# Performance work log

Hardware: AMD Instinct MI355X
Metric: run time of the kernel (lower is better)

Reference implementation:

```python
import jax, jax.numpy as jnp
import numpy as np
import math

S, B, D = 1024, 8, 512
H = 8
HD = D // H
DFF = 2048
NUM_BUCKETS = 32
MAX_DISTANCE = 128
LN_EPS = 1e-5


def setup_inputs() -> dict:
    key = jax.random.key(0)
    ks = jax.random.split(key, 12)
    s = 0.02
    return {
        "x": jax.random.normal(ks[0], (S, B, D), jnp.float32),
        "attn_mask": jnp.zeros((S, S), jnp.float32),
        "in_proj_w": jax.random.normal(ks[1], (3 * D, D), jnp.float32) * s,
        "in_proj_b": jnp.zeros((3 * D,), jnp.float32),
        "out_proj_w": jax.random.normal(ks[2], (D, D), jnp.float32) * s,
        "out_proj_b": jnp.zeros((D,), jnp.float32),
        "lin1_w": jax.random.normal(ks[3], (DFF, D), jnp.float32) * s,
        "lin1_b": jnp.zeros((DFF,), jnp.float32),
        "lin2_w": jax.random.normal(ks[4], (D, DFF), jnp.float32) * s,
        "lin2_b": jnp.zeros((D,), jnp.float32),
        "ln1_w": jnp.ones((D,), jnp.float32),
        "ln1_b": jnp.zeros((D,), jnp.float32),
        "ln2_w": jnp.ones((D,), jnp.float32),
        "ln2_b": jnp.zeros((D,), jnp.float32),
        "rel_emb": jax.random.normal(ks[5], (NUM_BUCKETS, H), jnp.float32) * s,
    }


def _relative_position_bucket(relative_position, num_buckets=NUM_BUCKETS, max_distance=MAX_DISTANCE):
    # bidirectional=True path (encoder)
    nb = num_buckets // 2
    rel_buckets = (relative_position > 0).astype(jnp.int32) * nb
    rp = jnp.abs(relative_position)
    max_exact = nb // 2
    is_small = rp < max_exact
    rp_safe = jnp.maximum(rp, 1)  # avoid log(0); masked by is_small below
    rp_large = max_exact + (
        jnp.log(rp_safe.astype(jnp.float32) / max_exact)
        / math.log(max_distance / max_exact)
        * (nb - max_exact)
    ).astype(jnp.int32)
    rp_large = jnp.minimum(rp_large, nb - 1)
    return rel_buckets + jnp.where(is_small, rp, rp_large)


def _compute_bias(rel_emb, q_len, k_len):
    ctx = jnp.arange(q_len, dtype=jnp.int32)[:, None]
    mem = jnp.arange(k_len, dtype=jnp.int32)[None, :]
    buckets = _relative_position_bucket(mem - ctx)          # [S, S]
    values = rel_emb[buckets]                                # [S, S, H]
    return jnp.transpose(values, (2, 0, 1))                  # [H, S, S]


def _layer_norm(x, w, b):
    mu = jnp.mean(x, axis=-1, keepdims=True)
    var = jnp.mean(jnp.square(x - mu), axis=-1, keepdims=True)
    return (x - mu) * jax.lax.rsqrt(var + LN_EPS) * w + b


def reference(x, attn_mask, in_proj_w, in_proj_b, out_proj_w, out_proj_b,
              lin1_w, lin1_b, lin2_w, lin2_b, ln1_w, ln1_b, ln2_w, ln2_b, rel_emb):
    s, b, d = x.shape
    # qkv projection (torch Linear: y = x W^T + b)
    qkv = x @ in_proj_w.T + in_proj_b                         # [S, B, 3D]
    q, k, v = jnp.split(qkv, 3, axis=-1)

    def to_bhsd(t):
        return jnp.transpose(t.reshape(s, b, H, HD), (1, 2, 0, 3))  # [B, H, S, HD]

    q, k, v = to_bhsd(q), to_bhsd(k), to_bhsd(v)
    scores = jnp.einsum("bhqd,bhkd->bhqk", q, k) / math.sqrt(HD)

    bias = _compute_bias(rel_emb, s, s)                       # [H, S, S]
    mask_bias = attn_mask[None, :, :] + bias                  # [H, S, S]
    attn = jax.nn.softmax(scores + mask_bias[None], axis=-1)  # [B, H, S, S]

    o = jnp.einsum("bhqk,bhkd->bhqd", attn, v)                # [B, H, S, HD]
    o = jnp.transpose(o, (2, 0, 1, 3)).reshape(s, b, d)       # [S, B, D]
    o = o @ out_proj_w.T + out_proj_b

    # post-norm (norm_first=False)
    y = _layer_norm(x + o, ln1_w, ln1_b)
    ff = jax.nn.relu(y @ lin1_w.T + lin1_b) @ lin2_w.T + lin2_b
    return _layer_norm(y + ff, ln2_w, ln2_b)
```

## Files before the change

### kernel.cpp

```cpp
#include <hip/hip_runtime.h>
#include <hip/hip_bf16.h>


#define S_LEN 1024
#define BATCH 8
#define DMODEL 512
#define NHEAD 8
#define HDIM 64
#define DFF 2048
#define NROWS (S_LEN * BATCH)

typedef __bf16 bf16x8 __attribute__((ext_vector_type(8)));
typedef float f32x4 __attribute__((ext_vector_type(4)));

__device__ __forceinline__ void gload16(const void* g, void* l) {
    __builtin_amdgcn_global_load_lds(
        (const __attribute__((address_space(1))) void*)g,
        (__attribute__((address_space(3))) void*)l, 16, 0, 0);
}

__global__ __launch_bounds__(256)
void cast_kernel(const float* __restrict__ in, __hip_bfloat16* __restrict__ out, int n) {
    int i = (blockIdx.x * blockDim.x + threadIdx.x) * 4;
    if (i + 3 < n) {
        float4 v = *(const float4*)(in + i);
        out[i + 0] = __float2bfloat16(v.x);
        out[i + 1] = __float2bfloat16(v.y);
        out[i + 2] = __float2bfloat16(v.z);
        out[i + 3] = __float2bfloat16(v.w);
    }
}

__global__ void bias_table_kernel(const float* __restrict__ rel_emb,
                                  float* __restrict__ bias_tab) {
    int idx = blockIdx.x * blockDim.x + threadIdx.x;
    if (idx >= 2 * S_LEN - 1) return;
    int rel = idx - (S_LEN - 1);
    int bucket = (rel > 0) ? 16 : 0;
    int rp = rel < 0 ? -rel : rel;
    int v;
    if (rp < 8)          v = rp;
    else if (rp < 12)    v = 8;
    else if (rp < 16)    v = 9;
    else if (rp < 23)    v = 10;
    else if (rp < 32)    v = 11;
    else if (rp < 46)    v = 12;
    else if (rp < 64)    v = 13;
    else if (rp < 91)    v = 14;
    else                 v = 15;
    bucket += v;
    for (int h = 0; h < NHEAD; ++h)
        bias_tab[idx * NHEAD + h] = rel_emb[bucket * NHEAD + h];
}

__global__ __launch_bounds__(256)
void embc_kernel(const float* __restrict__ mask,
                 const float* __restrict__ bias_tab,
                 __hip_bfloat16* __restrict__ embC) {
    int tid = blockIdx.x * 256 + threadIdx.x;
    int h  = tid >> 16;
    int r1 = tid & 65535;
    int qt = r1 >> 12;
    int w  = (r1 >> 10) & 3;
    int kb = (r1 >> 6) & 15;
    int lane = r1 & 63;
    int qbase = qt * 64 + w * 16 + (lane >> 4) * 4;
    int kbase = kb * 64 + (lane & 15);
    __hip_bfloat16 ov[16];
#pragma unroll
    for (int j = 0; j < 16; ++j) {
        int c = j >> 2, e = j & 3;
        int q = qbase + e, k = kbase + c * 16;
        float m = mask[(size_t)q * S_LEN + k];
        float bt = bias_tab[(k - q + S_LEN - 1) * NHEAD + h];
        ov[j] = __float2bfloat16(__expf(m + bt));
    }
    *(uint4*)(embC + (size_t)tid * 16) = *(uint4*)&ov[0];
    *(uint4*)(embC + (size_t)tid * 16 + 8) = *(uint4*)&ov[8];
}

template <int MODE, bool RELU, int NTILE>
__global__ __launch_bounds__(256)
void gemm_tile(const __hip_bfloat16* __restrict__ Ab,
               const __hip_bfloat16* __restrict__ Wb,
               const float* __restrict__ bias,
               void* __restrict__ outv,
               int N, int M, int K) {
    constexpr int RT = (NTILE == 128) ? 4 : 2;
    constexpr int NB = NTILE / 32;
    const int w = threadIdx.x >> 6;
    const int lane = threadIdx.x & 63;
    const int m16 = lane & 15;
    const int quad = lane >> 4;
    const int row0 = blockIdx.y * 128;
    const int col0 = blockIdx.x * NTILE;
    const int rowbase = (NTILE == 128) ? (w >> 1) * 64 : w * 32;
    const int colbase = (NTILE == 128) ? (w & 1) * 64 : 0;

    __shared__ __align__(16) __bf16 As[128 * 64];
    __shared__ __align__(16) __bf16 Bs[NTILE * 64];

    const __bf16* Ap = (const __bf16*)Ab;
    const __bf16* Wp = (const __bf16*)Wb;

    const int a_row_in_grp = lane >> 3;
    const int kb_sw = (lane & 7) ^ (lane >> 3);

    f32x4 acc[4][RT];
#pragma unroll
    for (int c = 0; c < 4; ++c)
#pragma unroll
        for (int r = 0; r < RT; ++r) acc[c][r] = f32x4{0, 0, 0, 0};

    for (int k0 = 0; k0 < K; k0 += 64) {
#pragma unroll
        for (int i = 0; i < 4; ++i) {
            int grp = w * 4 + i;
            int row = grp * 8 + a_row_in_grp;
            gload16(Ap + (size_t)(row0 + row) * K + k0 + kb_sw * 8,
                    (void*)(As + grp * 512));
        }
#pragma unroll
        for (int i = 0; i < NB; ++i) {
            int grp = w * NB + i;
            int row = grp * 8 + a_row_in_grp;
            gload16(Wp + (size_t)(col0 + row) * K + k0 + kb_sw * 8,
                    (void*)(Bs + grp * 512));
        }
        __syncthreads();

#pragma unroll
        for (int kk = 0; kk < 2; ++kk) {
            bf16x8 af[RT], bfr[4];
#pragma unroll
            for (int r = 0; r < RT; ++r) {
                int rr = rowbase + r * 16 + m16;
                int slot = (kk * 4 + quad) ^ (m16 & 7);
                af[r] = *(const bf16x8*)(As + rr * 64 + slot * 8);
            }
#pragma unroll
            for (int c = 0; c < 4; ++c) {
                int rr = colbase + c * 16 + m16;
                int slot = (kk * 4 + quad) ^ (m16 & 7);
                bfr[c] = *(const bf16x8*)(Bs + rr * 64 + slot * 8);
            }
#pragma unroll
            for (int c = 0; c < 4; ++c)
#pragma unroll
                for (int r = 0; r < RT; ++r)
                    acc[c][r] = __builtin_amdgcn_mfma_f32_16x16x32_bf16(
                        af[r], bfr[c], acc[c][r], 0, 0, 0);
        }
        __syncthreads();
    }

#pragma unroll
    for (int c = 0; c < 4; ++c) {
        int col = col0 + colbase + c * 16 + m16;
        float bv = bias[col];
#pragma unroll
        for (int r = 0; r < RT; ++r) {
#pragma unroll
            for (int e = 0; e < 4; ++e) {
                int row = row0 + rowbase + r * 16 + quad * 4 + e;
                float v = acc[c][r][e] + bv;
                if (RELU) v = fmaxf(v, 0.f);
                if (MODE == 0) {
                    ((float*)outv)[(size_t)row * M + col] = v;
                } else if (MODE == 1) {
                    ((__hip_bfloat16*)outv)[(size_t)row * M + col] = __float2bfloat16(v);
                } else {
                    int sect = col >> 9, h = (col >> 6) & 7, d = col & 63;
                    int s = row >> 3, bb = row & 7;
                    size_t idx;
                    if (sect == 2)
                        idx = (size_t)(128 + bb * 8 + h) * (S_LEN * HDIM)
                            + (size_t)d * S_LEN + s;
                    else
                        idx = ((size_t)(sect * 64 + bb * 8 + h) * S_LEN + s) * HDIM + d;
                    ((__hip_bfloat16*)outv)[idx] = __float2bfloat16(v);
                }
            }
        }
    }
}

__device__ __forceinline__ int p_addr(int r, int k) {
    return r * 64 + ((((k >> 3) ^ (r & 7))) << 3) + (k & 7);
}

__global__ __launch_bounds__(256, 4)
void attn_mfma(const __hip_bfloat16* __restrict__ qkv_bhsd,
               const __hip_bfloat16* __restrict__ embC,
               __hip_bfloat16* __restrict__ o) {
    const int bh = blockIdx.y;
    const int b = bh >> 3, h = bh & 7;
    const int qt = blockIdx.x;
    const int q0 = qt * 64;
    const int t = threadIdx.x;
    const int w = t >> 6, lane = t & 63, m16 = lane & 15, quad = lane >> 4;

    const __bf16* Qb  = (const __bf16*)qkv_bhsd + (size_t)bh * (S_LEN * HDIM);
    const __bf16* Kb  = (const __bf16*)qkv_bhsd + (size_t)(64 + bh) * (S_LEN * HDIM);
    const __bf16* VTg = (const __bf16*)qkv_bhsd + (size_t)(128 + bh) * (S_LEN * HDIM);
    const __hip_bfloat16* ec =
        embC + ((((size_t)h * 16 + qt) * 4 + w) * 16) * 1024 + (size_t)lane * 16;

    __shared__ __align__(16) __bf16 Ks[2][64 * 64];
    __shared__ __align__(16) __bf16 Vs[2][64 * 64];
    __shared__ __align__(16) __bf16 P[4][16 * 64];

    const int r_in = lane >> 3;
    const int kb_sw = (lane & 7) ^ r_in;

    auto stage = [&](int kc, int p) {
#pragma unroll
        for (int i = 0; i < 2; ++i) {
            int grp = w * 2 + i;
            gload16(Kb + (size_t)(kc + grp * 8 + r_in) * HDIM + kb_sw * 8,
                    (void*)(&Ks[p][grp * 512]));
            gload16(VTg + (size_t)(grp * 8 + r_in) * S_LEN + kc + kb_sw * 8,
                    (void*)(&Vs[p][grp * 512]));
        }
    };

    bf16x8 aQ0, aQ1;
    {
        const __bf16* qp = Qb + (size_t)(q0 + w * 16 + m16) * HDIM + quad * 8;
        bf16x8 t0 = *(const bf16x8*)qp;
        bf16x8 t1 = *(const bf16x8*)(qp + 32);
#pragma unroll
        for (int j = 0; j < 8; ++j) {
            t0[j] = (__bf16)((float)t0[j] * 0.125f);
            t1[j] = (__bf16)((float)t1[j] * 0.125f);
        }
        aQ0 = t0; aQ1 = t1;
    }

    f32x4 accO[4] = {f32x4{0,0,0,0}, f32x4{0,0,0,0}, f32x4{0,0,0,0}, f32x4{0,0,0,0}};
    float lpart[4] = {0.f, 0.f, 0.f, 0.f};

    stage(0, 0);
    __syncthreads();

    int p = 0;
    for (int kc = 0; kc < S_LEN; kc += 64, p ^= 1) {
        if (kc + 64 < S_LEN) stage(kc + 64, p ^ 1);

        union { uint4 u[2]; __hip_bfloat16 e[16]; } ev;
        ev.u[0] = *(const uint4*)(ec + (size_t)(kc >> 6) * 1024);
        ev.u[1] = *(const uint4*)(ec + (size_t)(kc >> 6) * 1024 + 8);

        f32x4 accS[4] = {f32x4{0,0,0,0}, f32x4{0,0,0,0}, f32x4{0,0,0,0}, f32x4{0,0,0,0}};
        const int sub = (m16 >> 3) * 512 + (m16 & 7) * 64;
        const int s0 = (quad ^ (m16 & 7)) * 8;
        const int s1 = ((4 + quad) ^ (m16 & 7)) * 8;
#pragma unroll
        for (int c = 0; c < 4; ++c) {
            const __bf16* kr = &Ks[p][c * 1024 + sub];
            bf16x8 b0 = *(const bf16x8*)(kr + s0);
            bf16x8 b1 = *(const bf16x8*)(kr + s1);
            accS[c] = __builtin_amdgcn_mfma_f32_16x16x32_bf16(aQ0, b0, accS[c], 0, 0, 0);
            accS[c] = __builtin_amdgcn_mfma_f32_16x16x32_bf16(aQ1, b1, accS[c], 0, 0, 0);
        }

#pragma unroll
        for (int c = 0; c < 4; ++c)
#pragma unroll
            for (int e = 0; e < 4; ++e) {
                float pv = __expf(accS[c][e]) * __bfloat162float(ev.e[c * 4 + e]);
                lpart[e] += pv;
                P[w][p_addr(quad * 4 + e, c * 16 + m16)] = (__bf16)pv;
            }

        bf16x8 aP0 = *(const bf16x8*)&P[w][p_addr(m16, quad * 8)];
        bf16x8 aP1 = *(const bf16x8*)&P[w][p_addr(m16, 32 + quad * 8)];
#pragma unroll
        for (int c = 0; c < 4; ++c) {
            const __bf16* vr = &Vs[p][c * 1024 + sub];
            bf16x8 v0 = *(const bf16x8*)(vr + s0);
            bf16x8 v1 = *(const bf16x8*)(vr + s1);
            accO[c] = __builtin_amdgcn_mfma_f32_16x16x32_bf16(aP0, v0, accO[c], 0, 0, 0);
            accO[c] = __builtin_amdgcn_mfma_f32_16x16x32_bf16(aP1, v1, accO[c], 0, 0, 0);
        }

        __syncthreads();
    }

    float lrow[4];
#pragma unroll
    for (int e = 0; e < 4; ++e) {
        float l = lpart[e];
#pragma unroll
        for (int off = 1; off < 16; off <<= 1) l += __shfl_xor(l, off);
        lrow[e] = 1.f / l;
    }

#pragma unroll
    for (int c = 0; c < 4; ++c)
#pragma unroll
        for (int e = 0; e < 4; ++e) {
            int row = q0 + w * 16 + quad * 4 + e;
            int d = c * 16 + m16;
            float v = accO[c][e] * lrow[e];
            o[((size_t)row * BATCH + b) * DMODEL + h * HDIM + d] = __float2bfloat16(v);
        }
}

__global__ __launch_bounds__(64)
void ln_kernel(const float* __restrict__ resid,
               const float* __restrict__ gin,
               const float* __restrict__ w,
               const float* __restrict__ b,
               float* __restrict__ outf,
               __hip_bfloat16* __restrict__ outb) {
    const int row = blockIdx.x;
    const int lane = threadIdx.x;
    const float* rp = resid + (size_t)row * DMODEL;
    const float* gp = gin + (size_t)row * DMODEL;

    float v[8];
    float s = 0.f, s2 = 0.f;
#pragma unroll
    for (int i = 0; i < 8; ++i) {
        int d = i * 64 + lane;
        float x = rp[d] + gp[d];
        v[i] = x;
        s += x;
        s2 += x * x;
    }
#pragma unroll
    for (int off = 32; off; off >>= 1) {
        s  += __shfl_xor(s, off);
        s2 += __shfl_xor(s2, off);
    }
    float mu = s * (1.f / DMODEL);
    float var = s2 * (1.f / DMODEL) - mu * mu;
    float rs = rsqrtf(var + 1e-5f);
#pragma unroll
    for (int i = 0; i < 8; ++i) {
        int d = i * 64 + lane;
        float y = (v[i] - mu) * rs * w[d] + b[d];
        outf[(size_t)row * DMODEL + d] = y;
        if (outb) outb[(size_t)row * DMODEL + d] = __float2bfloat16(y);
    }
}

extern "C" void kernel_launch(void* const* d_in, const int* in_sizes, int n_in,
                              void* d_out, int out_size, void* d_ws, size_t ws_size,
                              hipStream_t stream) {
    const float* x          = (const float*)d_in[0];
    const float* attn_mask  = (const float*)d_in[1];
    const float* in_proj_w  = (const float*)d_in[2];
    const float* in_proj_b  = (const float*)d_in[3];
    const float* out_proj_w = (const float*)d_in[4];
    const float* out_proj_b = (const float*)d_in[5];
    const float* lin1_w     = (const float*)d_in[6];
    const float* lin1_b     = (const float*)d_in[7];
    const float* lin2_w     = (const float*)d_in[8];
    const float* lin2_b     = (const float*)d_in[9];
    const float* ln1_w      = (const float*)d_in[10];
    const float* ln1_b      = (const float*)d_in[11];
    const float* ln2_w      = (const float*)d_in[12];
    const float* ln2_b      = (const float*)d_in[13];
    const float* rel_emb    = (const float*)d_in[14];

    char* ws = (char*)d_ws;
    size_t off = 0;
    auto alloc = [&](size_t bytes) {
        char* p = ws + off;
        off += (bytes + 255) / 256 * 256;
        return (void*)p;
    };
    float* bias_tab       = (float*)alloc((2 * S_LEN - 1) * NHEAD * 4);
    __hip_bfloat16* embt  = (__hip_bfloat16*)alloc((size_t)NHEAD * S_LEN * S_LEN * 2);
    __hip_bfloat16* wqkvb = (__hip_bfloat16*)alloc((size_t)3 * DMODEL * DMODEL * 2);
    __hip_bfloat16* wob   = (__hip_bfloat16*)alloc((size_t)DMODEL * DMODEL * 2);
    __hip_bfloat16* w1b   = (__hip_bfloat16*)alloc((size_t)DFF * DMODEL * 2);
    __hip_bfloat16* w2b   = (__hip_bfloat16*)alloc((size_t)DMODEL * DFF * 2);
    __hip_bfloat16* xb    = (__hip_bfloat16*)alloc((size_t)NROWS * DMODEL * 2);
    __hip_bfloat16* qkvb  = (__hip_bfloat16*)alloc((size_t)3 * 64 * S_LEN * HDIM * 2);
    __hip_bfloat16* o     = (__hip_bfloat16*)alloc((size_t)NROWS * DMODEL * 2);
    float* tmp            = (float*)alloc((size_t)NROWS * DMODEL * 4);
    float* yf             = (float*)alloc((size_t)NROWS * DMODEL * 4);
    __hip_bfloat16* yb    = (__hip_bfloat16*)alloc((size_t)NROWS * DMODEL * 2);
    __hip_bfloat16* ffb   = (__hip_bfloat16*)alloc((size_t)NROWS * DFF * 2);

    float* out = (float*)d_out;

    cast_kernel<<<dim3(3 * DMODEL * DMODEL / 1024), 256, 0, stream>>>(in_proj_w, wqkvb, 3 * DMODEL * DMODEL);
    cast_kernel<<<dim3(DMODEL * DMODEL / 1024), 256, 0, stream>>>(out_proj_w, wob, DMODEL * DMODEL);
    cast_kernel<<<dim3(DFF * DMODEL / 1024), 256, 0, stream>>>(lin1_w, w1b, DFF * DMODEL);
    cast_kernel<<<dim3(DMODEL * DFF / 1024), 256, 0, stream>>>(lin2_w, w2b, DMODEL * DFF);
    cast_kernel<<<dim3(NROWS * DMODEL / 1024), 256, 0, stream>>>(x, xb, NROWS * DMODEL);
    bias_table_kernel<<<dim3(8), 256, 0, stream>>>(rel_emb, bias_tab);
    embc_kernel<<<dim3(2048), 256, 0, stream>>>(attn_mask, bias_tab, embt);

    gemm_tile<2, false, 128><<<dim3(12, 64), 256, 0, stream>>>(
        xb, wqkvb, in_proj_b, qkvb, NROWS, 3 * DMODEL, DMODEL);

    attn_mfma<<<dim3(S_LEN / 64, BATCH * NHEAD), 256, 0, stream>>>(
        qkvb, embt, o);

    gemm_tile<0, false, 64><<<dim3(8, 64), 256, 0, stream>>>(
        o, wob, out_proj_b, tmp, NROWS, DMODEL, DMODEL);

    ln_kernel<<<dim3(NROWS), 64, 0, stream>>>(x, tmp, ln1_w, ln1_b, yf, yb);

    gemm_tile<1, true, 128><<<dim3(16, 64), 256, 0, stream>>>(
        yb, w1b, lin1_b, ffb, NROWS, DFF, DMODEL);

    gemm_tile<0, false, 64><<<dim3(8, 64), 256, 0, stream>>>(
        ffb, w2b, lin2_b, tmp, NROWS, DMODEL, DFF);

    ln_kernel<<<dim3(NROWS), 64, 0, stream>>>(yf, tmp, ln2_w, ln2_b, out, nullptr);
}
```

Measured before the change: 299.4 us.

## Fuse cast kernels, inline bias buckets, double-buffer narrow GEMMs, transpose attention MFMAs

Merges the five weight/input cast launches into one vectorized prep kernel and computes relative-position buckets directly inside the embC kernel, removing the bias table kernel. Adds a double-buffered 64-column GEMM for the out-projection and FFN2 so global-to-LDS loads overlap MFMA work. The attention kernel now computes transposed score and output tiles, so each lane owns one query row: the row-sum becomes a two-step shuffle, P writes are packed 4-wide, and output stores are vectorized. The double buffer doubles LDS use in the narrow GEMM, and the changed embC index mapping must still match the layout the attention kernel reads.

```diff
diff --git a/kernel.cpp b/kernel.cpp
--- a/kernel.cpp
+++ b/kernel.cpp
@@ -11,7 +11,8 @@
 #define NROWS (S_LEN * BATCH)
 
 typedef __bf16 bf16x8 __attribute__((ext_vector_type(8)));
-typedef float f32x4 __attribute__((ext_vector_type(4)));
+typedef short  s16x4  __attribute__((ext_vector_type(4)));
+typedef float  f32x4  __attribute__((ext_vector_type(4)));
 
 __device__ __forceinline__ void gload16(const void* g, void* l) {
     __builtin_amdgcn_global_load_lds(
@@ -20,42 +21,34 @@
 }
 
 __global__ __launch_bounds__(256)
-void cast_kernel(const float* __restrict__ in, __hip_bfloat16* __restrict__ out, int n) {
-    int i = (blockIdx.x * blockDim.x + threadIdx.x) * 4;
-    if (i + 3 < n) {
-        float4 v = *(const float4*)(in + i);
-        out[i + 0] = __float2bfloat16(v.x);
-        out[i + 1] = __float2bfloat16(v.y);
-        out[i + 2] = __float2bfloat16(v.z);
-        out[i + 3] = __float2bfloat16(v.w);
-    }
-}
-
-__global__ void bias_table_kernel(const float* __restrict__ rel_emb,
-                                  float* __restrict__ bias_tab) {
-    int idx = blockIdx.x * blockDim.x + threadIdx.x;
-    if (idx >= 2 * S_LEN - 1) return;
-    int rel = idx - (S_LEN - 1);
-    int bucket = (rel > 0) ? 16 : 0;
-    int rp = rel < 0 ? -rel : rel;
-    int v;
-    if (rp < 8)          v = rp;
-    else if (rp < 12)    v = 8;
-    else if (rp < 16)    v = 9;
-    else if (rp < 23)    v = 10;
-    else if (rp < 32)    v = 11;
-    else if (rp < 46)    v = 12;
-    else if (rp < 64)    v = 13;
-    else if (rp < 91)    v = 14;
-    else                 v = 15;
-    bucket += v;
-    for (int h = 0; h < NHEAD; ++h)
-        bias_tab[idx * NHEAD + h] = rel_emb[bucket * NHEAD + h];
+void prep_kernel(const float* __restrict__ x,
+                 const float* __restrict__ wq, const float* __restrict__ wo,
+                 const float* __restrict__ w1, const float* __restrict__ w2,
+                 __hip_bfloat16* __restrict__ xb, __hip_bfloat16* __restrict__ wqb,
+                 __hip_bfloat16* __restrict__ wob, __hip_bfloat16* __restrict__ w1b,
+                 __hip_bfloat16* __restrict__ w2b) {
+    const int NX = NROWS * DMODEL / 4;
+    const int NQ = 3 * DMODEL * DMODEL / 4;
+    const int NO = DMODEL * DMODEL / 4;
+    const int N1 = DFF * DMODEL / 4;
+    int i = blockIdx.x * 256 + threadIdx.x;
+    const float* src; __hip_bfloat16* dst; int off;
+    if (i < NX)                         { src = x;  dst = xb;  off = i; }
+    else if ((i -= NX) < NQ)            { src = wq; dst = wqb; off = i; }
+    else if ((i -= NQ) < NO)            { src = wo; dst = wob; off = i; }
+    else if ((i -= NO) < N1)            { src = w1; dst = w1b; off = i; }
+    else if ((i -= N1) < N1)            { src = w2; dst = w2b; off = i; }
+    else return;
+    float4 v = *(const float4*)(src + (size_t)off * 4);
+    union { s16x4 s; __hip_bfloat16 b[4]; } u;
+    u.b[0] = __float2bfloat16(v.x); u.b[1] = __float2bfloat16(v.y);
+    u.b[2] = __float2bfloat16(v.z); u.b[3] = __float2bfloat16(v.w);
+    *(s16x4*)(dst + (size_t)off * 4) = u.s;
 }
 
 __global__ __launch_bounds__(256)
 void embc_kernel(const float* __restrict__ mask,
-                 const float* __restrict__ bias_tab,
+                 const float* __restrict__ rel_emb,
                  __hip_bfloat16* __restrict__ embC) {
     int tid = blockIdx.x * 256 + threadIdx.x;
     int h  = tid >> 16;
@@ -64,41 +57,50 @@
     int w  = (r1 >> 10) & 3;
     int kb = (r1 >> 6) & 15;
     int lane = r1 & 63;
-    int qbase = qt * 64 + w * 16 + (lane >> 4) * 4;
-    int kbase = kb * 64 + (lane & 15);
+    int q = qt * 64 + w * 16 + (lane & 15);
     __hip_bfloat16 ov[16];
 #pragma unroll
     for (int j = 0; j < 16; ++j) {
         int c = j >> 2, e = j & 3;
-        int q = qbase + e, k = kbase + c * 16;
-        float m = mask[(size_t)q * S_LEN + k];
-        float bt = bias_tab[(k - q + S_LEN - 1) * NHEAD + h];
-        ov[j] = __float2bfloat16(__expf(m + bt));
+        int k = kb * 64 + c * 16 + (lane >> 4) * 4 + e;
+        int rel = k - q;
+        int bucket = (rel > 0) ? 16 : 0;
+        int rp = rel < 0 ? -rel : rel;
+        int v;
+        if (rp < 8)          v = rp;
+        else if (rp < 12)    v = 8;
+        else if (rp < 16)    v = 9;
+        else if (rp < 23)    v = 10;
+        else if (rp < 32)    v = 11;
+        else if (rp < 46)    v = 12;
+        else if (rp < 64)    v = 13;
+        else if (rp < 91)    v = 14;
+        else                 v = 15;
+        float bt = rel_emb[(bucket + v) * NHEAD + h];
+        ov[j] = __float2bfloat16(__expf(mask[(size_t)q * S_LEN + k] + bt));
     }
     *(uint4*)(embC + (size_t)tid * 16) = *(uint4*)&ov[0];
     *(uint4*)(embC + (size_t)tid * 16 + 8) = *(uint4*)&ov[8];
 }
 
-template <int MODE, bool RELU, int NTILE>
+template <int MODE, bool RELU>
 __global__ __launch_bounds__(256)
 void gemm_tile(const __hip_bfloat16* __restrict__ Ab,
                const __hip_bfloat16* __restrict__ Wb,
                const float* __restrict__ bias,
                void* __restrict__ outv,
                int N, int M, int K) {
-    constexpr int RT = (NTILE == 128) ? 4 : 2;
-    constexpr int NB = NTILE / 32;
     const int w = threadIdx.x >> 6;
     const int lane = threadIdx.x & 63;
     const int m16 = lane & 15;
     const int quad = lane >> 4;
     const int row0 = blockIdx.y * 128;
-    const int col0 = blockIdx.x * NTILE;
-    const int rowbase = (NTILE == 128) ? (w >> 1) * 64 : w * 32;
-    const int colbase = (NTILE == 128) ? (w & 1) * 64 : 0;
+    const int col0 = blockIdx.x * 128;
+    const int rowbase = (w >> 1) * 64;
+    const int colbase = (w & 1) * 64;
 
     __shared__ __align__(16) __bf16 As[128 * 64];
-    __shared__ __align__(16) __bf16 Bs[NTILE * 64];
+    __shared__ __align__(16) __bf16 Bs[128 * 64];
 
     const __bf16* Ap = (const __bf16*)Ab;
     const __bf16* Wp = (const __bf16*)Wb;
@@ -106,11 +108,11 @@
     const int a_row_in_grp = lane >> 3;
     const int kb_sw = (lane & 7) ^ (lane >> 3);
 
-    f32x4 acc[4][RT];
+    f32x4 acc[4][4];
 #pragma unroll
     for (int c = 0; c < 4; ++c)
 #pragma unroll
-        for (int r = 0; r < RT; ++r) acc[c][r] = f32x4{0, 0, 0, 0};
+        for (int r = 0; r < 4; ++r) acc[c][r] = f32x4{0, 0, 0, 0};
 
     for (int k0 = 0; k0 < K; k0 += 64) {
 #pragma unroll
@@ -119,11 +121,6 @@
             int row = grp * 8 + a_row_in_grp;
             gload16(Ap + (size_t)(row0 + row) * K + k0 + kb_sw * 8,
                     (void*)(As + grp * 512));
-        }
-#pragma unroll
-        for (int i = 0; i < NB; ++i) {
-            int grp = w * NB + i;
-            int row = grp * 8 + a_row_in_grp;
             gload16(Wp + (size_t)(col0 + row) * K + k0 + kb_sw * 8,
                     (void*)(Bs + grp * 512));
         }
@@ -131,23 +128,18 @@
 
 #pragma unroll
         for (int kk = 0; kk < 2; ++kk) {
-            bf16x8 af[RT], bfr[4];
-#pragma unroll
-            for (int r = 0; r < RT; ++r) {
-                int rr = rowbase + r * 16 + m16;
-                int slot = (kk * 4 + quad) ^ (m16 & 7);
-                af[r] = *(const bf16x8*)(As + rr * 64 + slot * 8);
-            }
-#pragma unroll
-            for (int c = 0; c < 4; ++c) {
-                int rr = colbase + c * 16 + m16;
-                int slot = (kk * 4 + quad) ^ (m16 & 7);
-                bfr[c] = *(const bf16x8*)(Bs + rr * 64 + slot * 8);
-            }
+            bf16x8 af[4], bfr[4];
+            int slot = (kk * 4 + quad) ^ (m16 & 7);
+#pragma unroll
+            for (int r = 0; r < 4; ++r)
+                af[r] = *(const bf16x8*)(As + (rowbase + r * 16 + m16) * 64 + slot * 8);
 #pragma unroll
             for (int c = 0; c < 4; ++c)
-#pragma unroll
-                for (int r = 0; r < RT; ++r)
+                bfr[c] = *(const bf16x8*)(Bs + (colbase + c * 16 + m16) * 64 + slot * 8);
+#pragma unroll
+            for (int c = 0; c < 4; ++c)
+#pragma unroll
+                for (int r = 0; r < 4; ++r)
                     acc[c][r] = __builtin_amdgcn_mfma_f32_16x16x32_bf16(
                         af[r], bfr[c], acc[c][r], 0, 0, 0);
         }
@@ -159,15 +151,13 @@
         int col = col0 + colbase + c * 16 + m16;
         float bv = bias[col];
 #pragma unroll
-        for (int r = 0; r < RT; ++r) {
+        for (int r = 0; r < 4; ++r) {
 #pragma unroll
             for (int e = 0; e < 4; ++e) {
                 int row = row0 + rowbase + r * 16 + quad * 4 + e;
                 float v = acc[c][r][e] + bv;
                 if (RELU) v = fmaxf(v, 0.f);
-                if (MODE == 0) {
-                    ((float*)outv)[(size_t)row * M + col] = v;
-                } else if (MODE == 1) {
+                if (MODE == 1) {
                     ((__hip_bfloat16*)outv)[(size_t)row * M + col] = __float2bfloat16(v);
                 } else {
                     int sect = col >> 9, h = (col >> 6) & 7, d = col & 63;
@@ -185,8 +175,90 @@
     }
 }
 
-__device__ __forceinline__ int p_addr(int r, int k) {
-    return r * 64 + ((((k >> 3) ^ (r & 7))) << 3) + (k & 7);
+__global__ __launch_bounds__(256)
+void gemm64_db(const __hip_bfloat16* __restrict__ Ab,
+               const __hip_bfloat16* __restrict__ Wb,
+               const float* __restrict__ bias,
+               float* __restrict__ outf,
+               int N, int M, int K) {
+    const int w = threadIdx.x >> 6;
+    const int lane = threadIdx.x & 63;
+    const int m16 = lane & 15;
+    const int quad = lane >> 4;
+    const int row0 = blockIdx.y * 128;
+    const int col0 = blockIdx.x * 64;
+    const int rowbase = w * 32;
+
+    __shared__ __align__(16) __bf16 As[2][128 * 64];
+    __shared__ __align__(16) __bf16 Bs[2][64 * 64];
+
+    const __bf16* Ap = (const __bf16*)Ab;
+    const __bf16* Wp = (const __bf16*)Wb;
+
+    const int a_row_in_grp = lane >> 3;
+    const int kb_sw = (lane & 7) ^ (lane >> 3);
+
+    auto stage = [&](int k0, int p) {
+#pragma unroll
+        for (int i = 0; i < 4; ++i) {
+            int grp = w * 4 + i;
+            int row = grp * 8 + a_row_in_grp;
+            gload16(Ap + (size_t)(row0 + row) * K + k0 + kb_sw * 8,
+                    (void*)(&As[p][grp * 512]));
+        }
+#pragma unroll
+        for (int i = 0; i < 2; ++i) {
+            int grp = w * 2 + i;
+            int row = grp * 8 + a_row_in_grp;
+            gload16(Wp + (size_t)(col0 + row) * K + k0 + kb_sw * 8,
+                    (void*)(&Bs[p][grp * 512]));
+        }
+    };
+
+    f32x4 acc[4][2];
+#pragma unroll
+    for (int c = 0; c < 4; ++c)
+#pragma unroll
+        for (int r = 0; r < 2; ++r) acc[c][r] = f32x4{0, 0, 0, 0};
+
+    stage(0, 0);
+    __syncthreads();
+
+    int p = 0;
+    for (int k0 = 0; k0 < K; k0 += 64, p ^= 1) {
+        if (k0 + 64 < K) stage(k0 + 64, p ^ 1);
+#pragma unroll
+        for (int kk = 0; kk < 2; ++kk) {
+            bf16x8 af[2], bfr[4];
+            int slot = (kk * 4 + quad) ^ (m16 & 7);
+#pragma unroll
+            for (int r = 0; r < 2; ++r)
+                af[r] = *(const bf16x8*)(&As[p][(rowbase + r * 16 + m16) * 64 + slot * 8]);
+#pragma unroll
+            for (int c = 0; c < 4; ++c)
+                bfr[c] = *(const bf16x8*)(&Bs[p][(c * 16 + m16) * 64 + slot * 8]);
+#pragma unroll
+            for (int c = 0; c < 4; ++c)
+#pragma unroll
+                for (int r = 0; r < 2; ++r)
+                    acc[c][r] = __builtin_amdgcn_mfma_f32_16x16x32_bf16(
+                        af[r], bfr[c], acc[c][r], 0, 0, 0);
+        }
+        __syncthreads();
+    }
+
+#pragma unroll
+    for (int c = 0; c < 4; ++c) {
+        int col = col0 + c * 16 + m16;
+        float bv = bias[col];
+#pragma unroll
+        for (int r = 0; r < 2; ++r)
+#pragma unroll
+            for (int e = 0; e < 4; ++e) {
+                int row = row0 + rowbase + r * 16 + quad * 4 + e;
+                outf[(size_t)row * M + col] = acc[c][r][e] + bv;
+            }
+    }
 }
 
 __global__ __launch_bounds__(256, 4)
@@ -237,8 +309,8 @@
         aQ0 = t0; aQ1 = t1;
     }
 
-    f32x4 accO[4] = {f32x4{0,0,0,0}, f32x4{0,0,0,0}, f32x4{0,0,0,0}, f32x4{0,0,0,0}};
-    float lpart[4] = {0.f, 0.f, 0.f, 0.f};
+    f32x4 accOT[4] = {f32x4{0,0,0,0}, f32x4{0,0,0,0}, f32x4{0,0,0,0}, f32x4{0,0,0,0}};
+    float lpart = 0.f;
 
     stage(0, 0);
     __syncthreads();
@@ -251,7 +323,7 @@
         ev.u[0] = *(const uint4*)(ec + (size_t)(kc >> 6) * 1024);
         ev.u[1] = *(const uint4*)(ec + (size_t)(kc >> 6) * 1024 + 8);
 
-        f32x4 accS[4] = {f32x4{0,0,0,0}, f32x4{0,0,0,0}, f32x4{0,0,0,0}, f32x4{0,0,0,0}};
+        f32x4 accT[4] = {f32x4{0,0,0,0}, f32x4{0,0,0,0}, f32x4{0,0,0,0}, f32x4{0,0,0,0}};
         const int sub = (m16 >> 3) * 512 + (m16 & 7) * 64;
         const int s0 = (quad ^ (m16 & 7)) * 8;
         const int s1 = ((4 + quad) ^ (m16 & 7)) * 8;
@@ -260,51 +332,55 @@
             const __bf16* kr = &Ks[p][c * 1024 + sub];
             bf16x8 b0 = *(const bf16x8*)(kr + s0);
             bf16x8 b1 = *(const bf16x8*)(kr + s1);
-            accS[c] = __builtin_amdgcn_mfma_f32_16x16x32_bf16(aQ0, b0, accS[c], 0, 0, 0);
-            accS[c] = __builtin_amdgcn_mfma_f32_16x16x32_bf16(aQ1, b1, accS[c], 0, 0, 0);
-        }
-
-#pragma unroll
-        for (int c = 0; c < 4; ++c)
+            accT[c] = __builtin_amdgcn_mfma_f32_16x16x32_bf16(b0, aQ0, accT[c], 0, 0, 0);
+            accT[c] = __builtin_amdgcn_mfma_f32_16x16x32_bf16(b1, aQ1, accT[c], 0, 0, 0);
+        }
+
+#pragma unroll
+        for (int c = 0; c < 4; ++c) {
+            union { s16x4 s; __hip_bfloat16 bb[4]; } u;
 #pragma unroll
             for (int e = 0; e < 4; ++e) {
-                float pv = __expf(accS[c][e]) * __bfloat162float(ev.e[c * 4 + e]);
-                lpart[e] += pv;
-                P[w][p_addr(quad * 4 + e, c * 16 + m16)] = (__bf16)pv;
+                float pv = __expf(accT[c][e]) * __bfloat162float(ev.e[c * 4 + e]);
+                lpart += pv;
+                u.bb[e] = __float2bfloat16(pv);
             }
-
-        bf16x8 aP0 = *(const bf16x8*)&P[w][p_addr(m16, quad * 8)];
-        bf16x8 aP1 = *(const bf16x8*)&P[w][p_addr(m16, 32 + quad * 8)];
-#pragma unroll
-        for (int c = 0; c < 4; ++c) {
-            const __bf16* vr = &Vs[p][c * 1024 + sub];
+            int blk = (c * 2 + (quad >> 1)) ^ (m16 & 7);
+            *(s16x4*)&P[w][m16 * 64 + blk * 8 + (quad & 1) * 4] = u.s;
+        }
+
+        bf16x8 pb0 = *(const bf16x8*)&P[w][m16 * 64 + ((quad) ^ (m16 & 7)) * 8];
+        bf16x8 pb1 = *(const bf16x8*)&P[w][m16 * 64 + ((4 + quad) ^ (m16 & 7)) * 8];
+
+#pragma unroll
+        for (int dt = 0; dt < 4; ++dt) {
+            const __bf16* vr = &Vs[p][dt * 1024 + sub];
             bf16x8 v0 = *(const bf16x8*)(vr + s0);
             bf16x8 v1 = *(const bf16x8*)(vr + s1);
-            accO[c] = __builtin_amdgcn_mfma_f32_16x16x32_bf16(aP0, v0, accO[c], 0, 0, 0);
-            accO[c] = __builtin_amdgcn_mfma_f32_16x16x32_bf16(aP1, v1, accO[c], 0, 0, 0);
+            accOT[dt] = __builtin_amdgcn_mfma_f32_16x16x32_bf16(v0, pb0, accOT[dt], 0, 0, 0);
+            accOT[dt] = __builtin_amdgcn_mfma_f32_16x16x32_bf16(v1, pb1, accOT[dt], 0, 0, 0);
         }
 
         __syncthreads();
     }
 
-    float lrow[4];
-#pragma unroll
-    for (int e = 0; e < 4; ++e) {
-        float l = lpart[e];
-#pragma unroll
-        for (int off = 1; off < 16; off <<= 1) l += __shfl_xor(l, off);
-        lrow[e] = 1.f / l;
-    }
-
-#pragma unroll
-    for (int c = 0; c < 4; ++c)
-#pragma unroll
-        for (int e = 0; e < 4; ++e) {
-            int row = q0 + w * 16 + quad * 4 + e;
-            int d = c * 16 + m16;
-            float v = accO[c][e] * lrow[e];
-            o[((size_t)row * BATCH + b) * DMODEL + h * HDIM + d] = __float2bfloat16(v);
-        }
+    float l = lpart;
+    l += __shfl_xor(l, 16);
+    l += __shfl_xor(l, 32);
+    float inv = 1.f / l;
+
+    {
+        int q = q0 + w * 16 + m16;
+        __hip_bfloat16* op = o + ((size_t)q * BATCH + b) * DMODEL + h * HDIM;
+#pragma unroll
+        for (int dt = 0; dt < 4; ++dt) {
+            union { s16x4 s; __hip_bfloat16 bb[4]; } u;
+#pragma unroll
+            for (int e = 0; e < 4; ++e)
+                u.bb[e] = __float2bfloat16(accOT[dt][e] * inv);
+            *(s16x4*)(op + dt * 16 + quad * 4) = u.s;
+        }
+    }
 }
 
 __global__ __launch_bounds__(64)
@@ -372,7 +448,6 @@
         off += (bytes + 255) / 256 * 256;
         return (void*)p;
     };
-    float* bias_tab       = (float*)alloc((2 * S_LEN - 1) * NHEAD * 4);
     __hip_bfloat16* embt  = (__hip_bfloat16*)alloc((size_t)NHEAD * S_LEN * S_LEN * 2);
     __hip_bfloat16* wqkvb = (__hip_bfloat16*)alloc((size_t)3 * DMODEL * DMODEL * 2);
     __hip_bfloat16* wob   = (__hip_bfloat16*)alloc((size_t)DMODEL * DMODEL * 2);
@@ -388,29 +463,25 @@
 
     float* out = (float*)d_out;
 
-    cast_kernel<<<dim3(3 * DMODEL * DMODEL / 1024), 256, 0, stream>>>(in_proj_w, wqkvb, 3 * DMODEL * DMODEL);
-    cast_kernel<<<dim3(DMODEL * DMODEL / 1024), 256, 0, stream>>>(out_proj_w, wob, DMODEL * DMODEL);
-    cast_kernel<<<dim3(DFF * DMODEL / 1024), 256, 0, stream>>>(lin1_w, w1b, DFF * DMODEL);
-    cast_kernel<<<dim3(DMODEL * DFF / 1024), 256, 0, stream>>>(lin2_w, w2b, DMODEL * DFF);
-    cast_kernel<<<dim3(NROWS * DMODEL / 1024), 256, 0, stream>>>(x, xb, NROWS * DMODEL);
-    bias_table_kernel<<<dim3(8), 256, 0, stream>>>(rel_emb, bias_tab);
-    embc_kernel<<<dim3(2048), 256, 0, stream>>>(attn_mask, bias_tab, embt);
-
-    gemm_tile<2, false, 128><<<dim3(12, 64), 256, 0, stream>>>(
+    prep_kernel<<<dim3(7168), 256, 0, stream>>>(
+        x, in_proj_w, out_proj_w, lin1_w, lin2_w, xb, wqkvb, wob, w1b, w2b);
+    embc_kernel<<<dim3(2048), 256, 0, stream>>>(attn_mask, rel_emb, embt);
+
+    gemm_tile<2, false><<<dim3(12, 64), 256, 0, stream>>>(
         xb, wqkvb, in_proj_b, qkvb, NROWS, 3 * DMODEL, DMODEL);
 
     attn_mfma<<<dim3(S_LEN / 64, BATCH * NHEAD), 256, 0, stream>>>(
         qkvb, embt, o);
 
-    gemm_tile<0, false, 64><<<dim3(8, 64), 256, 0, stream>>>(
+    gemm64_db<<<dim3(8, 64), 256, 0, stream>>>(
         o, wob, out_proj_b, tmp, NROWS, DMODEL, DMODEL);
 
     ln_kernel<<<dim3(NROWS), 64, 0, stream>>>(x, tmp, ln1_w, ln1_b, yf, yb);
 
-    gemm_tile<1, true, 128><<<dim3(16, 64), 256, 0, stream>>>(
+    gemm_tile<1, true><<<dim3(16, 64), 256, 0, stream>>>(
         yb, w1b, lin1_b, ffb, NROWS, DFF, DMODEL);
 
-    gemm_tile<0, false, 64><<<dim3(8, 64), 256, 0, stream>>>(
+    gemm64_db<<<dim3(8, 64), 256, 0, stream>>>(
         ffb, w2b, lin2_b, tmp, NROWS, DMODEL, DFF);
 
     ln_kernel<<<dim3(NROWS), 64, 0, stream>>>(yf, tmp, ln2_w, ln2_b, out, nullptr);
```

Result: faster. 292.4 us (-2.4%).
